# Kernel tuning notes

Measured on AMD Instinct MI355X. Metric: run time of the kernel, lower is better.

Reference implementation:

```python
import jax, jax.numpy as jnp
import numpy as np

N_OER, N_CONCEPT, N_CLASS = 100000, 20000, 1000
F_ENT, HID = 64, 128
E_SR, E_EP, E_COV, E_BEL = 200000, 400000, 400000, 100000
NEG_SLOPE = 0.2


def _edges(k, n_src, n_dst, e):
    k1, k2 = jax.random.split(k)
    return jnp.stack([jax.random.randint(k1, (e,), 0, n_src),
                      jax.random.randint(k2, (e,), 0, n_dst)]).astype(jnp.int32)


def setup_inputs() -> dict:
    key = jax.random.key(0)
    ks = jax.random.split(key, 24)
    s = 0.05  # small init scale for numerically stable attention logits
    inp = {
        'x_oer': jax.random.normal(ks[0], (N_OER, F_ENT), jnp.float32),
        'x_concept': jax.random.normal(ks[1], (N_CONCEPT, F_ENT), jnp.float32),
        'x_class': jax.random.normal(ks[2], (N_CLASS, F_ENT), jnp.float32),
        'e_oer': jax.random.uniform(ks[3], (N_OER, F_ENT), jnp.float32),
        'e_concept': jax.random.uniform(ks[4], (N_CONCEPT, F_ENT), jnp.float32),
        'e_class': jax.random.uniform(ks[5], (N_CLASS, F_ENT), jnp.float32),
        'W_lin': jax.random.normal(ks[6], (3, F_ENT, HID), jnp.float32) * s,
        'b_lin': jnp.zeros((3, HID), jnp.float32),
        'Wsrc': jax.random.normal(ks[7], (2, 5, HID, HID), jnp.float32) * s,
        'Wdst': jax.random.normal(ks[8], (2, 5, HID, HID), jnp.float32) * s,
        'att_src': jax.random.normal(ks[9], (2, 5, HID), jnp.float32) * s,
        'att_dst': jax.random.normal(ks[10], (2, 5, HID), jnp.float32) * s,
        'b_gat': jnp.zeros((2, 5, HID), jnp.float32),
        'W_cls': jax.random.normal(ks[11], (2 * (F_ENT + HID), 1), jnp.float32) * s,
        'b_cls': jnp.zeros((1,), jnp.float32),
        'ei_before_sr': _edges(ks[12], N_OER, N_OER, E_SR),
        'ei_covers': _edges(ks[14], N_OER, N_CONCEPT, E_COV),
        'ei_belongs': _edges(ks[15], N_CONCEPT, N_CLASS, E_BEL),
        'ei_rev_covers': _edges(ks[16], N_CONCEPT, N_OER, E_COV),
        'ei_rev_belongs': _edges(ks[17], N_CLASS, N_CONCEPT, E_BEL),
    }
    # before_ep edges guaranteed self-loop-free (PyG removes then re-adds self loops)
    k1, k2 = jax.random.split(ks[13])
    src = jax.random.randint(k1, (E_EP,), 0, N_OER)
    dst = (src + jax.random.randint(k2, (E_EP,), 1, N_OER)) % N_OER
    inp['ei_before_ep'] = jnp.stack([src, dst]).astype(jnp.int32)
    return inp


def _gat(x_src, x_dst, src, dst, Ws, Wd, a_s, a_d, b, n_dst):
    # PyG GATConv, heads=1: h = xW (no bias); alpha = softmax_dst(leaky_relu(a_s.h_s[i] + a_d.h_d[j]))
    h_s = x_src @ Ws                                   # [Ns, C]
    h_d = x_dst @ Wd                                   # [Nd, C]
    logit = jax.nn.leaky_relu((h_s @ a_s)[src] + (h_d @ a_d)[dst], NEG_SLOPE)  # [E]
    m = jax.ops.segment_max(logit, dst, num_segments=n_dst)
    ex = jnp.exp(logit - m[dst])
    denom = jax.ops.segment_sum(ex, dst, num_segments=n_dst)
    alpha = ex / denom[dst]
    out = jax.ops.segment_sum(h_s[src] * alpha[:, None], dst, num_segments=n_dst)
    return out + b


def _forward(x_oer, x_concept, x_class, e_oer, e_concept, e_class,
             W_lin, b_lin, Wsrc, Wdst, att_src, att_dst, b_gat, W_cls, b_cls,
             ei_before_sr, ei_before_ep, ei_covers, ei_belongs,
             ei_rev_covers, ei_rev_belongs):
    # per-node-type input projection of the random embeddings
    h_oer = e_oer @ W_lin[0] + b_lin[0]
    h_con = e_concept @ W_lin[1] + b_lin[1]
    h_cls = e_class @ W_lin[2] + b_lin[2]

    # add self loops for OER->OER 'before_ep' (add_self_loops=True)
    loop = jnp.arange(N_OER, dtype=jnp.int32)
    ep_src = jnp.concatenate([ei_before_ep[0], loop])
    ep_dst = jnp.concatenate([ei_before_ep[1], loop])

    for l in range(2):
        P = lambda r: (Wsrc[l, r], Wdst[l, r], att_src[l, r], att_dst[l, r], b_gat[l, r])
        o_ep = _gat(h_oer, h_oer, ep_src, ep_dst, *P(0), N_OER)
        o_cov = _gat(h_oer, h_con, ei_covers[0], ei_covers[1], *P(1), N_CONCEPT)
        o_bel = _gat(h_con, h_cls, ei_belongs[0], ei_belongs[1], *P(2), N_CLASS)
        o_rcov = _gat(h_con, h_oer, ei_rev_covers[0], ei_rev_covers[1], *P(3), N_OER)
        o_rbel = _gat(h_cls, h_con, ei_rev_belongs[0], ei_rev_belongs[1], *P(4), N_CONCEPT)
        # HeteroConv aggr='mean' over edge types per destination node type
        h_oer = (o_ep + o_rcov) * 0.5
        h_con = (o_cov + o_rbel) * 0.5
        h_cls = o_bel

    n_oer = jnp.concatenate([x_oer, h_oer], axis=1)          # [N_OER, F_ENT+HID]
    feat = jnp.concatenate([n_oer[ei_before_sr[0]], n_oer[ei_before_sr[1]]], axis=1)
    return (feat @ W_cls + b_cls)[:, 0]                      # [E_SR]


def reference(x_oer, x_concept, x_class, e_oer, e_concept, e_class,
              W_lin, b_lin, Wsrc, Wdst, att_src, att_dst, b_gat, W_cls, b_cls,
              ei_before_sr, ei_before_ep, ei_covers, ei_belongs,
              ei_rev_covers, ei_rev_belongs):
    return _forward(x_oer, x_concept, x_class, e_oer, e_concept, e_class,
                    W_lin, b_lin, Wsrc, Wdst, att_src, att_dst, b_gat, W_cls, b_cls,
                    ei_before_sr, ei_before_ep, ei_covers, ei_belongs,
                    ei_rev_covers, ei_rev_belongs)
```

## Files before the change

kernel.cpp:

```cpp
#include <hip/hip_runtime.h>
#include <hip/hip_bf16.h>

#define NOER 100000
#define NCON 20000
#define NCLS 1000
#define FENT 64
#define HID 128
#define ESR 200000
#define EEP 400000
#define ECOV 400000
#define EBEL 100000
#define NEG 0.2f
#define NB_TOT 121000

#define SL0 0
#define SL1 NOER
#define SL2 (2*NOER)
#define SL3 (2*NOER + NCON)
#define SL4 (2*NOER + 2*NCON)
#define SL_TOT (2*NOER + 2*NCON + NCLS)
#define DL0 0
#define DL1 NOER
#define DL2 (NOER + NCON)
#define DL3 (NOER + NCON + NCLS)
#define DL4 (2*NOER + NCON + NCLS)
#define DL_TOT (2*NOER + 2*NCON + NCLS)
#define EX_TOT 1500000
#define SCAN_B1 ((DL_TOT + 255) / 256)

#define BSH 9
#define BWID (1 << BSH)
#define NBUCK ((DL_TOT + BWID - 1) / BWID)
#define EPB 4096
#define ABLK ((EX_TOT + EPB - 1) / EPB)

#define NB_OER ((NOER + 127) / 128)
#define NB_CON ((NCON + 127) / 128)
#define NB_CLS ((NCLS + 127) / 128)

typedef unsigned short u16;
typedef unsigned int u32;
typedef short v8s __attribute__((ext_vector_type(8)));
typedef float v4f __attribute__((ext_vector_type(4)));
typedef u32 v4u __attribute__((ext_vector_type(4)));

__device__ __forceinline__ float b2f(u32 bits) { return __uint_as_float(bits << 16); }
__device__ __forceinline__ u16 f2b(float x) {
    __hip_bfloat16 h = __float2bfloat16(x);
    return *(u16*)&h;
}
__device__ __forceinline__ float wredsum(float p) {
#pragma unroll
    for (int off = 32; off; off >>= 1) p += __shfl_down(p, off);
    return p;
}

__device__ __forceinline__ void edge_decode(int e, const int* __restrict__ ep,
                                            const int* __restrict__ cov,
                                            const int* __restrict__ bel,
                                            const int* __restrict__ rcov,
                                            const int* __restrict__ rbel,
                                            int& s, int& g) {
    if (e < 500000) {
        if (e < EEP) { s = ep[e]; g = DL0 + ep[EEP + e]; }
        else { s = e - EEP; g = DL0 + s; }
    } else if (e < 900000)  { int i = e - 500000;  s = cov[i];  g = DL1 + cov[ECOV + i]; }
    else if (e < 1000000)   { int i = e - 900000;  s = bel[i];  g = DL2 + bel[EBEL + i]; }
    else if (e < 1400000)   { int i = e - 1000000; s = rcov[i]; g = DL3 + rcov[ECOV + i]; }
    else                    { int i = e - 1400000; s = rbel[i]; g = DL4 + rbel[EBEL + i]; }
}

__global__ __launch_bounds__(256) void k_cntA(const int* __restrict__ ep, const int* __restrict__ cov,
                                              const int* __restrict__ bel, const int* __restrict__ rcov,
                                              const int* __restrict__ rbel, int* __restrict__ counts,
                                              int* __restrict__ bhm) {
    __shared__ int lh[NBUCK];
    for (int i = threadIdx.x; i < NBUCK; i += 256) lh[i] = 0;
    __syncthreads();
    int e0 = blockIdx.x * EPB;
    for (int k = 0; k < EPB; k += 256) {
        int e = e0 + k + threadIdx.x;
        if (e < EX_TOT) {
            int s, g;
            edge_decode(e, ep, cov, bel, rcov, rbel, s, g);
            atomicAdd(counts + g, 1);
            atomicAdd(&lh[g >> BSH], 1);
        }
    }
    __syncthreads();
    for (int i = threadIdx.x; i < NBUCK; i += 256) bhm[i * ABLK + blockIdx.x] = lh[i];
}

__device__ __forceinline__ int deg_bin(int d) { int b = d > 63 ? 63 : d; return 63 - b; }

__global__ void k_scan1(const int* __restrict__ counts, int* __restrict__ part,
                        int* __restrict__ bsum, int* __restrict__ bh) {
    __shared__ int sm[256];
    __shared__ int lh[64];
    if (threadIdx.x < 64) lh[threadIdx.x] = 0;
    __syncthreads();
    int i = blockIdx.x * 256 + threadIdx.x;
    int v = (i < DL_TOT) ? counts[i] : 0;
    if (i < DL_TOT) atomicAdd(&lh[deg_bin(v)], 1);
    sm[threadIdx.x] = v;
    __syncthreads();
#pragma unroll
    for (int off = 1; off < 256; off <<= 1) {
        int x = (threadIdx.x >= off) ? sm[threadIdx.x - off] : 0;
        __syncthreads();
        sm[threadIdx.x] += x;
        __syncthreads();
    }
    if (i < DL_TOT) part[i] = sm[threadIdx.x];
    if (threadIdx.x == 255) bsum[blockIdx.x] = sm[255];
    if (threadIdx.x < 64) bh[threadIdx.x * SCAN_B1 + blockIdx.x] = lh[threadIdx.x];
}

__global__ void k_scan2(int* __restrict__ bsum) {
    __shared__ int sm[1024];
    int t = threadIdx.x;
    sm[t] = (t < SCAN_B1) ? bsum[t] : 0;
    __syncthreads();
#pragma unroll
    for (int off = 1; off < 1024; off <<= 1) {
        int x = (t >= off) ? sm[t - off] : 0;
        __syncthreads();
        sm[t] += x;
        __syncthreads();
    }
    if (t < SCAN_B1) bsum[t] = sm[t];
}

__global__ void k_scan3(const int* __restrict__ part, const int* __restrict__ bsum,
                        const int* __restrict__ counts, int* __restrict__ S,
                        int* __restrict__ cursor) {
    int i = blockIdx.x * 256 + threadIdx.x;
    if (i >= DL_TOT) return;
    int b = blockIdx.x;
    int s = part[i] + (b > 0 ? bsum[b - 1] : 0);
    S[i] = s;
    cursor[i] = s - counts[i];
}

__global__ void k_bscanA(const int* __restrict__ bhm, const int* __restrict__ cursor,
                         int* __restrict__ starts) {
    __shared__ int sm[256];
    __shared__ int carry;
    int u = blockIdx.x, t = threadIdx.x;
    if (t == 0) carry = 0;
    __syncthreads();
    int base = cursor[u << BSH];
    for (int c0 = 0; c0 < ABLK; c0 += 256) {
        int i = c0 + t;
        int v = (i < ABLK) ? bhm[u * ABLK + i] : 0;
        sm[t] = v;
        __syncthreads();
#pragma unroll
        for (int off = 1; off < 256; off <<= 1) {
            int x = (t >= off) ? sm[t - off] : 0;
            __syncthreads();
            sm[t] += x;
            __syncthreads();
        }
        if (i < ABLK) starts[u * ABLK + i] = base + carry + sm[t] - v;
        __syncthreads();
        if (t == 255) carry += sm[255];
        __syncthreads();
    }
}

__global__ __launch_bounds__(256) void k_bfillA(const int* __restrict__ ep, const int* __restrict__ cov,
                                                const int* __restrict__ bel, const int* __restrict__ rcov,
                                                const int* __restrict__ rbel,
                                                const int* __restrict__ starts, uint2* __restrict__ pairs) {
    __shared__ int lh[NBUCK];
    for (int i = threadIdx.x; i < NBUCK; i += 256) lh[i] = starts[i * ABLK + blockIdx.x];
    __syncthreads();
    int e0 = blockIdx.x * EPB;
    for (int k = 0; k < EPB; k += 256) {
        int e = e0 + k + threadIdx.x;
        if (e < EX_TOT) {
            int s, g;
            edge_decode(e, ep, cov, bel, rcov, rbel, s, g);
            int pos = atomicAdd(&lh[g >> BSH], 1);
            pairs[pos] = make_uint2((u32)s, (u32)g);
        }
    }
}

__global__ void k_fill2(const uint2* __restrict__ pairs, int* __restrict__ cursor,
                        int* __restrict__ csr) {
    int i = blockIdx.x * blockDim.x + threadIdx.x;
    if (i >= EX_TOT) return;
    uint2 p = pairs[i];
    int pos = atomicAdd(cursor + p.y, 1);
    csr[pos] = (int)p.x;
}

__global__ void k_bscan(const int* __restrict__ bh, int* __restrict__ boff,
                        int* __restrict__ bintot) {
    __shared__ int sm[256];
    __shared__ int carry;
    int bin = blockIdx.x;
    if (threadIdx.x == 0) carry = 0;
    __syncthreads();
    for (int c0 = 0; c0 < SCAN_B1; c0 += 256) {
        int i = c0 + threadIdx.x;
        int v = (i < SCAN_B1) ? bh[bin * SCAN_B1 + i] : 0;
        sm[threadIdx.x] = v;
        __syncthreads();
#pragma unroll
        for (int off = 1; off < 256; off <<= 1) {
            int x = (threadIdx.x >= off) ? sm[threadIdx.x - off] : 0;
            __syncthreads();
            sm[threadIdx.x] += x;
            __syncthreads();
        }
        if (i < SCAN_B1) boff[bin * SCAN_B1 + i] = carry + sm[threadIdx.x] - v;
        __syncthreads();
        if (threadIdx.x == 255) carry += sm[255];
        __syncthreads();
    }
    if (threadIdx.x == 0) bintot[bin] = carry;
}

__global__ void k_hscan(const int* __restrict__ hist, int* __restrict__ bcur) {
    int t = threadIdx.x;
    int h = hist[t];
    int v = h;
#pragma unroll
    for (int off = 1; off < 64; off <<= 1) {
        int x = __shfl_up(v, off);
        if (t >= off) v += x;
    }
    bcur[t] = v - h;
}

__global__ void k_perm2(const int* __restrict__ counts, const int* __restrict__ binbase,
                        const int* __restrict__ boff, const int* __restrict__ S,
                        int* __restrict__ perm, int* __restrict__ segbeg,
                        int* __restrict__ segend) {
    __shared__ int lh[64];
    if (threadIdx.x < 64)
        lh[threadIdx.x] = binbase[threadIdx.x] + boff[threadIdx.x * SCAN_B1 + blockIdx.x];
    __syncthreads();
    int g = blockIdx.x * 256 + threadIdx.x;
    if (g >= DL_TOT) return;
    int c = counts[g];
    int se = S[g];
    int pos = atomicAdd(&lh[deg_bin(c)], 1);
    perm[pos] = g;
    segbeg[pos] = se - c;
    segend[pos] = se;
}

__global__ void k_cast(const float* __restrict__ e_oer, const float* __restrict__ e_con,
                       const float* __restrict__ e_cls, u16* __restrict__ eb) {
    int idx = blockIdx.x * blockDim.x + threadIdx.x;
    int i4 = idx * 4;
    if (i4 >= NB_TOT * FENT) return;
    const float* src;
    if (i4 < 6400000) src = e_oer + i4;
    else if (i4 < 7680000) src = e_con + (i4 - 6400000);
    else src = e_cls + (i4 - 7680000);
    float4 v = *(const float4*)src;
    u16* d = eb + i4;
    d[0] = f2b(v.x); d[1] = f2b(v.y); d[2] = f2b(v.z); d[3] = f2b(v.w);
}

__global__ void k_prep(const float* __restrict__ W_lin, const float* __restrict__ Wsrc,
                       const float* __restrict__ b_gat,
                       u16* __restrict__ Wlt, u16* __restrict__ Woer, u16* __restrict__ Wcon,
                       u16* __restrict__ Wcls, float* __restrict__ boer,
                       float* __restrict__ bcon, float* __restrict__ bcls2) {
    int i = blockIdx.x * 256 + threadIdx.x;
    if (i < 24576) {
        int t = i / 8192, r = i % 8192, c = r >> 6, k = r & 63;
        Wlt[i] = f2b(W_lin[t * 8192 + k * 128 + c]);
        return;
    }
    i -= 24576;
    if (i < 65536) {
        int l = i >> 15, r = i & 32767, c = r >> 8, k2 = r & 255;
        int rel = 5 * l + (k2 < 128 ? 0 : 3), k = k2 & 127;
        Woer[i] = f2b(Wsrc[(size_t)rel * 16384 + k * 128 + c]);
        return;
    }
    i -= 65536;
    if (i < 65536) {
        int l = i >> 15, r = i & 32767, c = r >> 8, k2 = r & 255;
        int rel = 5 * l + (k2 < 128 ? 1 : 4), k = k2 & 127;
        Wcon[i] = f2b(Wsrc[(size_t)rel * 16384 + k * 128 + c]);
        return;
    }
    i -= 65536;
    if (i < 32768) {
        int l = i >> 14, r = i & 16383, c = r >> 7, k = r & 127;
        Wcls[i] = f2b(Wsrc[(size_t)(5 * l + 2) * 16384 + k * 128 + c]);
        return;
    }
    i -= 32768;
    if (i < 256) { int l = i >> 7, c = i & 127;
        boer[i] = 0.5f * (b_gat[(5 * l + 0) * 128 + c] + b_gat[(5 * l + 3) * 128 + c]); return; }
    i -= 256;
    if (i < 256) { int l = i >> 7, c = i & 127;
        bcon[i] = 0.5f * (b_gat[(5 * l + 1) * 128 + c] + b_gat[(5 * l + 4) * 128 + c]); return; }
    i -= 256;
    if (i < 256) { int l = i >> 7, c = i & 127;
        bcls2[i] = b_gat[(5 * l + 2) * 128 + c]; }
}

__global__ void k_wvec(const float* __restrict__ Wsrc, const float* __restrict__ as_,
                       const float* __restrict__ Wdst, const float* __restrict__ ad,
                       float* __restrict__ wsv, float* __restrict__ wdv) {
    int a = blockIdx.x >> 5;
    int r = ((blockIdx.x & 31) << 2) + (threadIdx.x >> 6);
    int lane = threadIdx.x & 63;
    const float *W, *v;
    float* o;
    if (a < 10) { W = Wsrc + (size_t)a * HID * HID; v = as_ + a * HID; o = wsv + a * HID; }
    else { W = Wdst + (size_t)(a - 10) * HID * HID; v = ad + (a - 10) * HID; o = wdv + (a - 10) * HID; }
    float p = W[r * HID + lane] * v[lane] + W[r * HID + 64 + lane] * v[64 + lane];
    p = wredsum(p);
    if (lane == 0) o[r] = p;
}

struct GemmJob {
    const u16* A0;
    const u16* A1;
    const u16* Wt;
    const float* bias;
    float scale;
    int n, K;
    u16* out;
    const float* dv0; const float* dv1; const float* dv2; const float* dv3;
    float* do0; float* do1; float* do2; float* do3;
};

__global__ __launch_bounds__(256) void k_mgemm(GemmJob j0, GemmJob j1, GemmJob j2,
                                               int nb0, int nb1) {
    __shared__ u16 lA[128][40];
    __shared__ u16 lB[128][40];
    __shared__ float dvs[4][HID];
    __shared__ float pdot[128][4];
    GemmJob J;
    int b = blockIdx.x;
    if (b < nb0) J = j0;
    else if (b < nb0 + nb1) { J = j1; b -= nb0; }
    else { J = j2; b -= nb0 + nb1; }
    const int row0 = b * 128;
    const int tid = threadIdx.x, lane = tid & 63, w = tid >> 6;
    const int wr = w >> 1, wc = w & 1;
    const int fr = lane & 15, kg = lane >> 4;
    const int astride = J.A1 ? 128 : J.K;
    const bool dots = (J.do0 != nullptr);
    if (dots) {
        for (int i = tid; i < 4 * HID; i += 256) {
            int v = i >> 7, c = i & 127;
            const float* dv = (v == 0) ? J.dv0 : (v == 1) ? J.dv1 : (v == 2) ? J.dv2 : J.dv3;
            dvs[v][c] = dv ? dv[c] : 0.f;
        }
        for (int i = tid; i < 128 * 4; i += 256) ((float*)pdot)[i] = 0.f;
    }
    v4f acc[4][4];
#pragma unroll
    for (int i = 0; i < 4; ++i)
#pragma unroll
        for (int c = 0; c < 4; ++c) acc[i][c] = (v4f){0.f, 0.f, 0.f, 0.f};

    for (int k0 = 0; k0 < J.K; k0 += 32) {
        const u16* Asrc; int kk;
        if (k0 < 128) { Asrc = J.A0; kk = k0; } else { Asrc = J.A1; kk = k0 - 128; }
        __syncthreads();
#pragma unroll
        for (int p = 0; p < 2; ++p) {
            int m = tid + p * 256;
            int r = m >> 2, seg = m & 3;
            int gr = row0 + r;
            uint4 u = make_uint4(0u, 0u, 0u, 0u);
            if (gr < J.n) u = *(const uint4*)(Asrc + (size_t)gr * astride + kk + seg * 8);
            *(uint4*)&lA[r][seg * 8] = u;
        }
#pragma unroll
        for (int i = 0; i < 2; ++i) {
            int m = tid * 2 + i, c = m >> 2, seg = m & 3;
            uint4 u = *(const uint4*)(J.Wt + (size_t)c * J.K + k0 + seg * 8);
            *(uint4*)&lB[c][seg * 8] = u;
        }
        __syncthreads();
        v8s a[4];
#pragma unroll
        for (int i = 0; i < 4; ++i) a[i] = *(const v8s*)&lA[64 * wr + 16 * i + fr][8 * kg];
#pragma unroll
        for (int c = 0; c < 4; ++c) {
            v8s bf = *(const v8s*)&lB[64 * wc + 16 * c + fr][8 * kg];
#pragma unroll
            for (int i = 0; i < 4; ++i)
                acc[i][c] = __builtin_amdgcn_mfma_f32_16x16x32_bf16(a[i], bf, acc[i][c], 0, 0, 0);
        }
    }
#pragma unroll
    for (int i = 0; i < 4; ++i)
#pragma unroll
        for (int c = 0; c < 4; ++c) {
            int col = 64 * wc + 16 * c + fr;
            float bv = J.bias[col];
#pragma unroll
            for (int jj = 0; jj < 4; ++jj) {
                int gr = row0 + 64 * wr + 16 * i + 4 * kg + jj;
                if (gr < J.n) J.out[(size_t)gr * 128 + col] = f2b(acc[i][c][jj] * J.scale + bv);
            }
        }
    if (dots) {
#pragma unroll
        for (int i = 0; i < 4; ++i)
#pragma unroll
            for (int jj = 0; jj < 4; ++jj) {
                int rl = 64 * wr + 16 * i + 4 * kg + jj;
                float hv[4];
#pragma unroll
                for (int c = 0; c < 4; ++c)
                    hv[c] = acc[i][c][jj] * J.scale + J.bias[64 * wc + 16 * c + fr];
#pragma unroll
                for (int v = 0; v < 4; ++v) {
                    float p = 0.f;
#pragma unroll
                    for (int c = 0; c < 4; ++c)
                        p = fmaf(hv[c], dvs[v][64 * wc + 16 * c + fr], p);
                    p += __shfl_xor(p, 1);
                    p += __shfl_xor(p, 2);
                    p += __shfl_xor(p, 4);
                    p += __shfl_xor(p, 8);
                    if (fr == 0) atomicAdd(&pdot[rl][v], p);
                }
            }
        __syncthreads();
        if (tid < 128) {
            int gr = row0 + tid;
            if (gr < J.n) {
                if (J.do0) J.do0[gr] = pdot[tid][0];
                if (J.do1) J.do1[gr] = pdot[tid][1];
                if (J.do2) J.do2[gr] = pdot[tid][2];
                if (J.do3) J.do3[gr] = pdot[tid][3];
            }
        }
    }
}

__global__ __launch_bounds__(256) void k_agg_all(const int* __restrict__ csr,
                                                 const int* __restrict__ perm,
                                                 const int* __restrict__ segbeg,
                                                 const int* __restrict__ segend,
                                                 const float* __restrict__ slp,
                                                 const float* __restrict__ dlp,
                                                 const u16* __restrict__ hb,
                                                 u16* __restrict__ tmp) {
    int gi = blockIdx.x * 16 + (threadIdx.x >> 4);
    if (gi >= DL_TOT) return;
    int g = perm[gi];
    int beg = segbeg[gi];
    int end = segend[gi];
    int lane = threadIdx.x & 63;
    int ks = lane & 15;
    int grpbase = lane & 48;
    int c4 = ks * 4;
    const u32* h;
    int sb;
    if (g < DL1)      { h = (const u32*)hb; sb = SL0; }
    else if (g < DL2) { h = (const u32*)hb; sb = SL1; }
    else if (g < DL3) { h = (const u32*)(hb + (size_t)NOER * HID); sb = SL2; }
    else if (g < DL4) { h = (const u32*)(hb + (size_t)NOER * HID); sb = SL3; }
    else              { h = (const u32*)(hb + (size_t)(NOER + NCON) * HID); sb = SL4; }
    float dlv = dlp[g];
    const u32* hc = h + c4;
    float acc[8] = {};
    float denp = 0.f;
    for (int c0 = beg; c0 < end; c0 += 16) {
        int nch = end - c0;
        if (nch > 16) nch = 16;
        int s_l = 0;
        float ex_l = 0.f;
        if (ks < nch) {
            s_l = csr[c0 + ks];
            float lg = slp[sb + s_l] + dlv;
            lg = lg > 0.f ? lg : NEG * lg;
            ex_l = __expf(lg);
            denp += ex_l;
        }
        uint4 hu[16];
#pragma unroll
        for (int j = 0; j < 16; ++j) {
            if (j < nch) {
                int s = __shfl(s_l, grpbase + j);
                hu[j] = *(const uint4*)(hc + ((size_t)s << 6));
            }
        }
#pragma unroll
        for (int j = 0; j < 16; ++j) {
            if (j < nch) {
                float ex = __shfl(ex_l, grpbase + j);
#pragma unroll
                for (int q = 0; q < 4; ++q) {
                    u32 w = ((const u32*)&hu[j])[q];
                    acc[2 * q]     = fmaf(ex, __uint_as_float(w << 16), acc[2 * q]);
                    acc[2 * q + 1] = fmaf(ex, __uint_as_float(w & 0xffff0000u), acc[2 * q + 1]);
                }
            }
        }
    }
    denp += __shfl_xor(denp, 8);
    denp += __shfl_xor(denp, 4);
    denp += __shfl_xor(denp, 2);
    denp += __shfl_xor(denp, 1);
    float inv = (end > beg) ? 1.f / denp : 0.f;
    v4u r;
    r.x = (u32)f2b(acc[0] * inv) | ((u32)f2b(acc[1] * inv) << 16);
    r.y = (u32)f2b(acc[2] * inv) | ((u32)f2b(acc[3] * inv) << 16);
    r.z = (u32)f2b(acc[4] * inv) | ((u32)f2b(acc[5] * inv) << 16);
    r.w = (u32)f2b(acc[6] * inv) | ((u32)f2b(acc[7] * inv) << 16);
    __builtin_nontemporal_store(r, (v4u*)((u32*)tmp + (size_t)g * 64 + c4));
}

__global__ void k_score(const float* __restrict__ x, const u16* __restrict__ hb,
                        const float* __restrict__ Wc, float* __restrict__ s1,
                        float* __restrict__ s2) {
    int t = blockIdx.x * blockDim.x + threadIdx.x;
    int n = t >> 6, lane = t & 63;
    if (n >= NOER) return;
    float xv = x[(size_t)n * FENT + lane];
    u32 hu = ((const u32*)hb)[(size_t)n * 64 + lane];
    float h0 = b2f(hu & 0xffffu), h1 = b2f(hu >> 16);
    float2 wa = *(const float2*)(Wc + 64 + 2 * lane);
    float2 wb = *(const float2*)(Wc + 256 + 2 * lane);
    float p1 = xv * Wc[lane] + h0 * wa.x + h1 * wa.y;
    float p2 = xv * Wc[192 + lane] + h0 * wb.x + h1 * wb.y;
#pragma unroll
    for (int off = 32; off; off >>= 1) { p1 += __shfl_down(p1, off); p2 += __shfl_down(p2, off); }
    if (lane == 0) { s1[n] = p1; s2[n] = p2; }
}

__global__ void k_final(const int* __restrict__ src, const int* __restrict__ dst,
                        const float* __restrict__ s1, const float* __restrict__ s2,
                        const float* __restrict__ bcls, float* __restrict__ out) {
    int e = blockIdx.x * blockDim.x + threadIdx.x;
    if (e >= ESR) return;
    out[e] = s1[src[e]] + s2[dst[e]] + bcls[0];
}

extern "C" void kernel_launch(void* const* d_in, const int* in_sizes, int n_in,
                              void* d_out, int out_size, void* d_ws, size_t ws_size,
                              hipStream_t stream) {
    const float* x_oer   = (const float*)d_in[0];
    const float* e_oer   = (const float*)d_in[3];
    const float* e_con   = (const float*)d_in[4];
    const float* e_cls   = (const float*)d_in[5];
    const float* W_lin   = (const float*)d_in[6];
    const float* b_lin   = (const float*)d_in[7];
    const float* Wsrc    = (const float*)d_in[8];
    const float* Wdst    = (const float*)d_in[9];
    const float* att_src = (const float*)d_in[10];
    const float* att_dst = (const float*)d_in[11];
    const float* b_gat   = (const float*)d_in[12];
    const float* W_cls   = (const float*)d_in[13];
    const float* b_cls   = (const float*)d_in[14];
    const int* ei_sr   = (const int*)d_in[15];
    const int* ei_cov  = (const int*)d_in[16];
    const int* ei_bel  = (const int*)d_in[17];
    const int* ei_rcov = (const int*)d_in[18];
    const int* ei_rbel = (const int*)d_in[19];
    const int* ei_ep   = (const int*)d_in[20];

    float* ws = (float*)d_ws;
    size_t o = 0;
    u16* hb  = (u16*)(ws + o); o += (size_t)NB_TOT * HID / 2;
    u16* eb  = (u16*)(ws + o); o += (size_t)NB_TOT * FENT / 2;
    u16* tmp = (u16*)(ws + o); o += (size_t)DL_TOT * HID / 2;
    float* slp  = ws + o; o += SL_TOT;
    float* dlp  = ws + o; o += DL_TOT;
    float* wsv  = ws + o; o += 10 * HID;
    float* wdv  = ws + o; o += 10 * HID;
    u16* Wlt  = (u16*)(ws + o); o += 3 * HID * FENT / 2;
    u16* Woer = (u16*)(ws + o); o += 2 * HID * 256 / 2;
    u16* Wcon = (u16*)(ws + o); o += 2 * HID * 256 / 2;
    u16* Wcls = (u16*)(ws + o); o += 2 * HID * HID / 2;
    float* boerb = ws + o; o += 2 * HID;
    float* bconb = ws + o; o += 2 * HID;
    float* bcls2 = ws + o; o += 2 * HID;
    float* s1 = ws + o; o += NOER;
    float* s2 = ws + o; o += NOER;
    int* counts = (int*)(ws + o); o += DL_TOT;
    int* part   = (int*)(ws + o); o += DL_TOT;
    int* S      = (int*)(ws + o); o += DL_TOT;
    int* cursor = (int*)(ws + o); o += DL_TOT;
    int* perm   = (int*)(ws + o); o += DL_TOT;
    int* segbeg = (int*)(ws + o); o += DL_TOT;
    int* segend = (int*)(ws + o); o += DL_TOT;
    int* bsum   = (int*)(ws + o); o += 1024;
    int* bhm    = (int*)(ws + o); o += NBUCK * ABLK;
    int* starts = (int*)(ws + o); o += NBUCK * ABLK;
    int* bh     = (int*)(ws + o); o += 64 * SCAN_B1;
    int* boff   = (int*)(ws + o); o += 64 * SCAN_B1;
    int* bintot = (int*)(ws + o); o += 64;
    int* binbase= (int*)(ws + o); o += 64;
    uint2* pairs = (uint2*)(ws + o); o += (size_t)EX_TOT * 2;
    int* csr    = (int*)(ws + o); o += EX_TOT;

    u16* hb_con = hb + (size_t)NOER * HID;
    u16* hb_cls = hb + (size_t)(NOER + NCON) * HID;

    hipMemsetAsync(counts, 0, DL_TOT * sizeof(int), stream);
    k_cntA<<<ABLK, 256, 0, stream>>>(ei_ep, ei_cov, ei_bel, ei_rcov, ei_rbel, counts, bhm);
    k_scan1<<<SCAN_B1, 256, 0, stream>>>(counts, part, bsum, bh);
    k_scan2<<<1, 1024, 0, stream>>>(bsum);
    k_scan3<<<SCAN_B1, 256, 0, stream>>>(part, bsum, counts, S, cursor);
    k_bscanA<<<NBUCK, 256, 0, stream>>>(bhm, cursor, starts);
    k_bfillA<<<ABLK, 256, 0, stream>>>(ei_ep, ei_cov, ei_bel, ei_rcov, ei_rbel, starts, pairs);
    k_fill2<<<(EX_TOT + 255) / 256, 256, 0, stream>>>(pairs, cursor, csr);
    k_bscan<<<64, 256, 0, stream>>>(bh, boff, bintot);
    k_hscan<<<1, 64, 0, stream>>>(bintot, binbase);
    k_perm2<<<SCAN_B1, 256, 0, stream>>>(counts, binbase, boff, S, perm, segbeg, segend);

    k_prep<<<739, 256, 0, stream>>>(W_lin, Wsrc, b_gat, Wlt, Woer, Wcon, Wcls, boerb, bconb, bcls2);
    k_cast<<<(NB_TOT * FENT / 4 + 255) / 256, 256, 0, stream>>>(e_oer, e_con, e_cls, eb);
    k_wvec<<<640, 256, 0, stream>>>(Wsrc, att_src, Wdst, att_dst, wsv, wdv);

    const int NBT = NB_OER + NB_CON + NB_CLS;

    {
        GemmJob ja = {eb, nullptr, Wlt, b_lin, 1.f, NOER, FENT, hb,
                      wsv + 0 * HID, wsv + 1 * HID, wdv + 0 * HID, wdv + 3 * HID,
                      slp + SL0, slp + SL1, dlp + DL0, dlp + DL3};
        GemmJob jb = {eb + (size_t)NOER * FENT, nullptr, Wlt + 8192, b_lin + 128, 1.f, NCON, FENT, hb_con,
                      wsv + 2 * HID, wsv + 3 * HID, wdv + 1 * HID, wdv + 4 * HID,
                      slp + SL2, slp + SL3, dlp + DL1, dlp + DL4};
        GemmJob jc = {eb + (size_t)(NOER + NCON) * FENT, nullptr, Wlt + 16384, b_lin + 256, 1.f, NCLS, FENT, hb_cls,
                      wsv + 4 * HID, wdv + 2 * HID, nullptr, nullptr,
                      slp + SL4, dlp + DL2, nullptr, nullptr};
        k_mgemm<<<NBT, 256, 0, stream>>>(ja, jb, jc, NB_OER, NB_CON);
    }

    for (int l = 0; l < 2; ++l) {
        k_agg_all<<<(DL_TOT + 15) / 16, 256, 0, stream>>>(csr, perm, segbeg, segend, slp, dlp, hb, tmp);
        int nb = (l + 1) * 5;
        bool nd = (l == 0);
        GemmJob ja = {tmp + (size_t)DL0 * HID, tmp + (size_t)DL3 * HID,
                      Woer + l * 32768, boerb + l * HID, 0.5f, NOER, 256, hb,
                      nd ? wsv + (nb + 0) * HID : nullptr, nd ? wsv + (nb + 1) * HID : nullptr,
                      nd ? wdv + (nb + 0) * HID : nullptr, nd ? wdv + (nb + 3) * HID : nullptr,
                      nd ? slp + SL0 : nullptr, nd ? slp + SL1 : nullptr,
                      nd ? dlp + DL0 : nullptr, nd ? dlp + DL3 : nullptr};
        GemmJob jb = {tmp + (size_t)DL1 * HID, tmp + (size_t)DL4 * HID,
                      Wcon + l * 32768, bconb + l * HID, 0.5f, NCON, 256, hb_con,
                      nd ? wsv + (nb + 2) * HID : nullptr, nd ? wsv + (nb + 3) * HID : nullptr,
                      nd ? wdv + (nb + 1) * HID : nullptr, nd ? wdv + (nb + 4) * HID : nullptr,
                      nd ? slp + SL2 : nullptr, nd ? slp + SL3 : nullptr,
                      nd ? dlp + DL1 : nullptr, nd ? dlp + DL4 : nullptr};
        GemmJob jc = {tmp + (size_t)DL2 * HID, nullptr,
                      Wcls + l * 16384, bcls2 + l * HID, 1.f, NCLS, 128, hb_cls,
                      nd ? wsv + (nb + 4) * HID : nullptr, nd ? wdv + (nb + 2) * HID : nullptr,
                      nullptr, nullptr,
                      nd ? slp + SL4 : nullptr, nd ? dlp + DL2 : nullptr, nullptr, nullptr};
        k_mgemm<<<NBT, 256, 0, stream>>>(ja, jb, jc, NB_OER, NB_CON);
    }

    k_score<<<(NOER * 64 + 255) / 256, 256, 0, stream>>>(x_oer, hb, W_cls, s1, s2);
    k_final<<<(ESR + 255) / 256, 256, 0, stream>>>(ei_sr, ei_sr + ESR, s1, s2, b_cls, (float*)d_out);
}
```

Measured before the change: 465.2 us.

## Merge prep kernels into one launch and fuse classifier dot into last GEMM epilogue

The edge-count, embedding cast, weight-prep and attention-vector kernels are merged into a single multi-role launch, which removes launch gaps and lets independent work overlap. The second-layer GEMM epilogue now computes the hidden-part classifier dots (W_cls slices) into s1h/s2h through the existing attention-logit hook, so k_score no longer rereads the bf16 hidden features. Non-temporal loads are added for the pairs and csr streams. The fused epilogue changes the hidden rounding path and relies on the GEMM epilogue computing a plain dot product with those vectors.

```diff
diff --git a/kernel.cpp b/kernel.cpp
--- a/kernel.cpp
+++ b/kernel.cpp
@@ -38,6 +38,12 @@
 #define NB_CON ((NCON + 127) / 128)
 #define NB_CLS ((NCLS + 127) / 128)
 
+#define CAST_BLKS ((NB_TOT * FENT / 4 + 255) / 256)
+#define MISC_B0 ABLK
+#define MISC_B1 (MISC_B0 + CAST_BLKS)
+#define MISC_B2 (MISC_B1 + 739)
+#define MISC_B3 (MISC_B2 + 640)
+
 typedef unsigned short u16;
 typedef unsigned int u32;
 typedef short v8s __attribute__((ext_vector_type(8)));
@@ -70,25 +76,103 @@
     else                    { int i = e - 1400000; s = rbel[i]; g = DL4 + rbel[EBEL + i]; }
 }
 
-__global__ __launch_bounds__(256) void k_cntA(const int* __restrict__ ep, const int* __restrict__ cov,
+__global__ __launch_bounds__(256) void k_misc(const int* __restrict__ ep, const int* __restrict__ cov,
                                               const int* __restrict__ bel, const int* __restrict__ rcov,
                                               const int* __restrict__ rbel, int* __restrict__ counts,
-                                              int* __restrict__ bhm) {
+                                              int* __restrict__ bhm,
+                                              const float* __restrict__ e_oer, const float* __restrict__ e_con,
+                                              const float* __restrict__ e_cls, u16* __restrict__ eb,
+                                              const float* __restrict__ W_lin, const float* __restrict__ Wsrc,
+                                              const float* __restrict__ b_gat,
+                                              u16* __restrict__ Wlt, u16* __restrict__ Woer, u16* __restrict__ Wcon,
+                                              u16* __restrict__ Wcls, float* __restrict__ boer,
+                                              float* __restrict__ bcon, float* __restrict__ bcls2,
+                                              const float* __restrict__ as_, const float* __restrict__ Wdst,
+                                              const float* __restrict__ ad,
+                                              float* __restrict__ wsv, float* __restrict__ wdv) {
     __shared__ int lh[NBUCK];
-    for (int i = threadIdx.x; i < NBUCK; i += 256) lh[i] = 0;
-    __syncthreads();
-    int e0 = blockIdx.x * EPB;
-    for (int k = 0; k < EPB; k += 256) {
-        int e = e0 + k + threadIdx.x;
-        if (e < EX_TOT) {
-            int s, g;
-            edge_decode(e, ep, cov, bel, rcov, rbel, s, g);
-            atomicAdd(counts + g, 1);
-            atomicAdd(&lh[g >> BSH], 1);
-        }
-    }
-    __syncthreads();
-    for (int i = threadIdx.x; i < NBUCK; i += 256) bhm[i * ABLK + blockIdx.x] = lh[i];
+    int blk = blockIdx.x;
+    if (blk < MISC_B0) {
+        for (int i = threadIdx.x; i < NBUCK; i += 256) lh[i] = 0;
+        __syncthreads();
+        int e0 = blk * EPB;
+        for (int k = 0; k < EPB; k += 256) {
+            int e = e0 + k + threadIdx.x;
+            if (e < EX_TOT) {
+                int s, g;
+                edge_decode(e, ep, cov, bel, rcov, rbel, s, g);
+                atomicAdd(counts + g, 1);
+                atomicAdd(&lh[g >> BSH], 1);
+            }
+        }
+        __syncthreads();
+        for (int i = threadIdx.x; i < NBUCK; i += 256) bhm[i * ABLK + blk] = lh[i];
+        return;
+    }
+    if (blk < MISC_B1) {
+        int idx = (blk - MISC_B0) * 256 + threadIdx.x;
+        int i4 = idx * 4;
+        if (i4 >= NB_TOT * FENT) return;
+        const float* src;
+        if (i4 < 6400000) src = e_oer + i4;
+        else if (i4 < 7680000) src = e_con + (i4 - 6400000);
+        else src = e_cls + (i4 - 7680000);
+        float4 v = *(const float4*)src;
+        u16* d = eb + i4;
+        d[0] = f2b(v.x); d[1] = f2b(v.y); d[2] = f2b(v.z); d[3] = f2b(v.w);
+        return;
+    }
+    if (blk < MISC_B2) {
+        int i = (blk - MISC_B1) * 256 + threadIdx.x;
+        if (i < 24576) {
+            int t = i / 8192, r = i % 8192, c = r >> 6, k = r & 63;
+            Wlt[i] = f2b(W_lin[t * 8192 + k * 128 + c]);
+            return;
+        }
+        i -= 24576;
+        if (i < 65536) {
+            int l = i >> 15, r = i & 32767, c = r >> 8, k2 = r & 255;
+            int rel = 5 * l + (k2 < 128 ? 0 : 3), k = k2 & 127;
+            Woer[i] = f2b(Wsrc[(size_t)rel * 16384 + k * 128 + c]);
+            return;
+        }
+        i -= 65536;
+        if (i < 65536) {
+            int l = i >> 15, r = i & 32767, c = r >> 8, k2 = r & 255;
+            int rel = 5 * l + (k2 < 128 ? 1 : 4), k = k2 & 127;
+            Wcon[i] = f2b(Wsrc[(size_t)rel * 16384 + k * 128 + c]);
+            return;
+        }
+        i -= 65536;
+        if (i < 32768) {
+            int l = i >> 14, r = i & 16383, c = r >> 7, k = r & 127;
+            Wcls[i] = f2b(Wsrc[(size_t)(5 * l + 2) * 16384 + k * 128 + c]);
+            return;
+        }
+        i -= 32768;
+        if (i < 256) { int l = i >> 7, c = i & 127;
+            boer[i] = 0.5f * (b_gat[(5 * l + 0) * 128 + c] + b_gat[(5 * l + 3) * 128 + c]); return; }
+        i -= 256;
+        if (i < 256) { int l = i >> 7, c = i & 127;
+            bcon[i] = 0.5f * (b_gat[(5 * l + 1) * 128 + c] + b_gat[(5 * l + 4) * 128 + c]); return; }
+        i -= 256;
+        if (i < 256) { int l = i >> 7, c = i & 127;
+            bcls2[i] = b_gat[(5 * l + 2) * 128 + c]; }
+        return;
+    }
+    {
+        int bb = blk - MISC_B2;
+        int a = bb >> 5;
+        int r = ((bb & 31) << 2) + (threadIdx.x >> 6);
+        int lane = threadIdx.x & 63;
+        const float *W, *v;
+        float* o;
+        if (a < 10) { W = Wsrc + (size_t)a * HID * HID; v = as_ + a * HID; o = wsv + a * HID; }
+        else { W = Wdst + (size_t)(a - 10) * HID * HID; v = ad + (a - 10) * HID; o = wdv + (a - 10) * HID; }
+        float p = W[r * HID + lane] * v[lane] + W[r * HID + 64 + lane] * v[64 + lane];
+        p = wredsum(p);
+        if (lane == 0) o[r] = p;
+    }
 }
 
 __device__ __forceinline__ int deg_bin(int d) { int b = d > 63 ? 63 : d; return 63 - b; }
@@ -192,9 +276,10 @@
                         int* __restrict__ csr) {
     int i = blockIdx.x * blockDim.x + threadIdx.x;
     if (i >= EX_TOT) return;
-    uint2 p = pairs[i];
-    int pos = atomicAdd(cursor + p.y, 1);
-    csr[pos] = (int)p.x;
+    u32 px = __builtin_nontemporal_load(&pairs[i].x);
+    u32 py = __builtin_nontemporal_load(&pairs[i].y);
+    int pos = atomicAdd(cursor + py, 1);
+    csr[pos] = (int)px;
 }
 
 __global__ void k_bscan(const int* __restrict__ bh, int* __restrict__ boff,
@@ -252,77 +337,6 @@
     perm[pos] = g;
     segbeg[pos] = se - c;
     segend[pos] = se;
-}
-
-__global__ void k_cast(const float* __restrict__ e_oer, const float* __restrict__ e_con,
-                       const float* __restrict__ e_cls, u16* __restrict__ eb) {
-    int idx = blockIdx.x * blockDim.x + threadIdx.x;
-    int i4 = idx * 4;
-    if (i4 >= NB_TOT * FENT) return;
-    const float* src;
-    if (i4 < 6400000) src = e_oer + i4;
-    else if (i4 < 7680000) src = e_con + (i4 - 6400000);
-    else src = e_cls + (i4 - 7680000);
-    float4 v = *(const float4*)src;
-    u16* d = eb + i4;
-    d[0] = f2b(v.x); d[1] = f2b(v.y); d[2] = f2b(v.z); d[3] = f2b(v.w);
-}
-
-__global__ void k_prep(const float* __restrict__ W_lin, const float* __restrict__ Wsrc,
-                       const float* __restrict__ b_gat,
-                       u16* __restrict__ Wlt, u16* __restrict__ Woer, u16* __restrict__ Wcon,
-                       u16* __restrict__ Wcls, float* __restrict__ boer,
-                       float* __restrict__ bcon, float* __restrict__ bcls2) {
-    int i = blockIdx.x * 256 + threadIdx.x;
-    if (i < 24576) {
-        int t = i / 8192, r = i % 8192, c = r >> 6, k = r & 63;
-        Wlt[i] = f2b(W_lin[t * 8192 + k * 128 + c]);
-        return;
-    }
-    i -= 24576;
-    if (i < 65536) {
-        int l = i >> 15, r = i & 32767, c = r >> 8, k2 = r & 255;
-        int rel = 5 * l + (k2 < 128 ? 0 : 3), k = k2 & 127;
-        Woer[i] = f2b(Wsrc[(size_t)rel * 16384 + k * 128 + c]);
-        return;
-    }
-    i -= 65536;
-    if (i < 65536) {
-        int l = i >> 15, r = i & 32767, c = r >> 8, k2 = r & 255;
-        int rel = 5 * l + (k2 < 128 ? 1 : 4), k = k2 & 127;
-        Wcon[i] = f2b(Wsrc[(size_t)rel * 16384 + k * 128 + c]);
-        return;
-    }
-    i -= 65536;
-    if (i < 32768) {
-        int l = i >> 14, r = i & 16383, c = r >> 7, k = r & 127;
-        Wcls[i] = f2b(Wsrc[(size_t)(5 * l + 2) * 16384 + k * 128 + c]);
-        return;
-    }
-    i -= 32768;
-    if (i < 256) { int l = i >> 7, c = i & 127;
-        boer[i] = 0.5f * (b_gat[(5 * l + 0) * 128 + c] + b_gat[(5 * l + 3) * 128 + c]); return; }
-    i -= 256;
-    if (i < 256) { int l = i >> 7, c = i & 127;
-        bcon[i] = 0.5f * (b_gat[(5 * l + 1) * 128 + c] + b_gat[(5 * l + 4) * 128 + c]); return; }
-    i -= 256;
-    if (i < 256) { int l = i >> 7, c = i & 127;
-        bcls2[i] = b_gat[(5 * l + 2) * 128 + c]; }
-}
-
-__global__ void k_wvec(const float* __restrict__ Wsrc, const float* __restrict__ as_,
-                       const float* __restrict__ Wdst, const float* __restrict__ ad,
-                       float* __restrict__ wsv, float* __restrict__ wdv) {
-    int a = blockIdx.x >> 5;
-    int r = ((blockIdx.x & 31) << 2) + (threadIdx.x >> 6);
-    int lane = threadIdx.x & 63;
-    const float *W, *v;
-    float* o;
-    if (a < 10) { W = Wsrc + (size_t)a * HID * HID; v = as_ + a * HID; o = wsv + a * HID; }
-    else { W = Wdst + (size_t)(a - 10) * HID * HID; v = ad + (a - 10) * HID; o = wdv + (a - 10) * HID; }
-    float p = W[r * HID + lane] * v[lane] + W[r * HID + 64 + lane] * v[64 + lane];
-    p = wredsum(p);
-    if (lane == 0) o[r] = p;
 }
 
 struct GemmJob {
@@ -481,7 +495,7 @@
         int s_l = 0;
         float ex_l = 0.f;
         if (ks < nch) {
-            s_l = csr[c0 + ks];
+            s_l = __builtin_nontemporal_load(&csr[c0 + ks]);
             float lg = slp[sb + s_l] + dlv;
             lg = lg > 0.f ? lg : NEG * lg;
             ex_l = __expf(lg);
@@ -521,22 +535,18 @@
     __builtin_nontemporal_store(r, (v4u*)((u32*)tmp + (size_t)g * 64 + c4));
 }
 
-__global__ void k_score(const float* __restrict__ x, const u16* __restrict__ hb,
-                        const float* __restrict__ Wc, float* __restrict__ s1,
-                        float* __restrict__ s2) {
+__global__ void k_score(const float* __restrict__ x, const float* __restrict__ s1h,
+                        const float* __restrict__ s2h, const float* __restrict__ Wc,
+                        float* __restrict__ s1, float* __restrict__ s2) {
     int t = blockIdx.x * blockDim.x + threadIdx.x;
     int n = t >> 6, lane = t & 63;
     if (n >= NOER) return;
     float xv = x[(size_t)n * FENT + lane];
-    u32 hu = ((const u32*)hb)[(size_t)n * 64 + lane];
-    float h0 = b2f(hu & 0xffffu), h1 = b2f(hu >> 16);
-    float2 wa = *(const float2*)(Wc + 64 + 2 * lane);
-    float2 wb = *(const float2*)(Wc + 256 + 2 * lane);
-    float p1 = xv * Wc[lane] + h0 * wa.x + h1 * wa.y;
-    float p2 = xv * Wc[192 + lane] + h0 * wb.x + h1 * wb.y;
+    float p1 = xv * Wc[lane];
+    float p2 = xv * Wc[192 + lane];
 #pragma unroll
     for (int off = 32; off; off >>= 1) { p1 += __shfl_down(p1, off); p2 += __shfl_down(p2, off); }
-    if (lane == 0) { s1[n] = p1; s2[n] = p2; }
+    if (lane == 0) { s1[n] = p1 + s1h[n]; s2[n] = p2 + s2h[n]; }
 }
 
 __global__ void k_final(const int* __restrict__ src, const int* __restrict__ dst,
@@ -588,6 +598,8 @@
     float* bcls2 = ws + o; o += 2 * HID;
     float* s1 = ws + o; o += NOER;
     float* s2 = ws + o; o += NOER;
+    float* s1h = ws + o; o += NOER;
+    float* s2h = ws + o; o += NOER;
     int* counts = (int*)(ws + o); o += DL_TOT;
     int* part   = (int*)(ws + o); o += DL_TOT;
     int* S      = (int*)(ws + o); o += DL_TOT;
@@ -609,7 +621,11 @@
     u16* hb_cls = hb + (size_t)(NOER + NCON) * HID;
 
     hipMemsetAsync(counts, 0, DL_TOT * sizeof(int), stream);
-    k_cntA<<<ABLK, 256, 0, stream>>>(ei_ep, ei_cov, ei_bel, ei_rcov, ei_rbel, counts, bhm);
+    k_misc<<<MISC_B3, 256, 0, stream>>>(ei_ep, ei_cov, ei_bel, ei_rcov, ei_rbel, counts, bhm,
+                                        e_oer, e_con, e_cls, eb,
+                                        W_lin, Wsrc, b_gat, Wlt, Woer, Wcon, Wcls,
+                                        boerb, bconb, bcls2,
+                                        att_src, Wdst, att_dst, wsv, wdv);
     k_scan1<<<SCAN_B1, 256, 0, stream>>>(counts, part, bsum, bh);
     k_scan2<<<1, 1024, 0, stream>>>(bsum);
     k_scan3<<<SCAN_B1, 256, 0, stream>>>(part, bsum, counts, S, cursor);
@@ -619,10 +635,6 @@
     k_bscan<<<64, 256, 0, stream>>>(bh, boff, bintot);
     k_hscan<<<1, 64, 0, stream>>>(bintot, binbase);
     k_perm2<<<SCAN_B1, 256, 0, stream>>>(counts, binbase, boff, S, perm, segbeg, segend);
-
-    k_prep<<<739, 256, 0, stream>>>(W_lin, Wsrc, b_gat, Wlt, Woer, Wcon, Wcls, boerb, bconb, bcls2);
-    k_cast<<<(NB_TOT * FENT / 4 + 255) / 256, 256, 0, stream>>>(e_oer, e_con, e_cls, eb);
-    k_wvec<<<640, 256, 0, stream>>>(Wsrc, att_src, Wdst, att_dst, wsv, wdv);
 
     const int NBT = NB_OER + NB_CON + NB_CLS;
 
@@ -641,13 +653,15 @@
 
     for (int l = 0; l < 2; ++l) {
         k_agg_all<<<(DL_TOT + 15) / 16, 256, 0, stream>>>(csr, perm, segbeg, segend, slp, dlp, hb, tmp);
-        int nb = (l + 1) * 5;
         bool nd = (l == 0);
+        int nb = 5;
         GemmJob ja = {tmp + (size_t)DL0 * HID, tmp + (size_t)DL3 * HID,
                       Woer + l * 32768, boerb + l * HID, 0.5f, NOER, 256, hb,
-                      nd ? wsv + (nb + 0) * HID : nullptr, nd ? wsv + (nb + 1) * HID : nullptr,
-                      nd ? wdv + (nb + 0) * HID : nullptr, nd ? wdv + (nb + 3) * HID : nullptr,
-                      nd ? slp + SL0 : nullptr, nd ? slp + SL1 : nullptr,
+                      nd ? wsv + (nb + 0) * HID : W_cls + 64,
+                      nd ? wsv + (nb + 1) * HID : W_cls + 256,
+                      nd ? wdv + (nb + 0) * HID : nullptr,
+                      nd ? wdv + (nb + 3) * HID : nullptr,
+                      nd ? slp + SL0 : s1h, nd ? slp + SL1 : s2h,
                       nd ? dlp + DL0 : nullptr, nd ? dlp + DL3 : nullptr};
         GemmJob jb = {tmp + (size_t)DL1 * HID, tmp + (size_t)DL4 * HID,
                       Wcon + l * 32768, bconb + l * HID, 0.5f, NCON, 256, hb_con,
@@ -663,6 +677,6 @@
         k_mgemm<<<NBT, 256, 0, stream>>>(ja, jb, jc, NB_OER, NB_CON);
     }
 
-    k_score<<<(NOER * 64 + 255) / 256, 256, 0, stream>>>(x_oer, hb, W_cls, s1, s2);
+    k_score<<<(NOER * 64 + 255) / 256, 256, 0, stream>>>(x_oer, s1h, s2h, W_cls, s1, s2);
     k_final<<<(ESR + 255) / 256, 256, 0, stream>>>(ei_sr, ei_sr + ESR, s1, s2, b_cls, (float*)d_out);
 }
```

Result: slower. 485.2 us (+4.3%).
